# Kernel tuning notes

Measured on AMD Instinct MI355X. Metric: run time of the kernel, lower is better.

The kernel has to match this reference:

```python
import jax, jax.numpy as jnp
import numpy as np
import math

N_NODES = 100000
D = 64
N_EDGES = 1280000
LN_EPS = 1e-5


def setup_inputs() -> dict:
    key = jax.random.key(0)
    ks = jax.random.split(key, 8)
    x = jax.random.normal(ks[0], (N_NODES, D), dtype=jnp.float32)
    edge_index = jax.random.randint(ks[1], (2, N_EDGES), 0, N_NODES, dtype=jnp.int64)
    # xavier_uniform with gain=0.1 for weight matrices
    limit = 0.1 * math.sqrt(6.0 / (D + D))
    qk_w = jax.random.uniform(ks[2], (D, D), dtype=jnp.float32, minval=-limit, maxval=limit)
    v_w = jax.random.uniform(ks[3], (D, D), dtype=jnp.float32, minval=-limit, maxval=limit)
    o_w = jax.random.uniform(ks[4], (D, D), dtype=jnp.float32, minval=-limit, maxval=limit)
    qk_b = jnp.zeros((D,), dtype=jnp.float32)
    v_b = jnp.zeros((D,), dtype=jnp.float32)
    o_b = jnp.zeros((D,), dtype=jnp.float32)
    ln_g = jnp.ones((D,), dtype=jnp.float32)
    ln_b = jnp.zeros((D,), dtype=jnp.float32)
    return {"x": x, "edge_index": edge_index, "qk_w": qk_w, "qk_b": qk_b,
            "v_w": v_w, "v_b": v_b, "o_w": o_w, "o_b": o_b,
            "ln_g": ln_g, "ln_b": ln_b}


def reference(x, edge_index, qk_w, qk_b, v_w, v_b, o_w, o_b, ln_g, ln_b):
    n = x.shape[0]
    # shared Q/K projection and V projection (torch Linear: x @ W^T + b)
    qk = x @ qk_w.T + qk_b            # [N, D]
    v = x @ v_w.T + v_b               # [N, D]

    src = edge_index[0]
    dst = edge_index[1]

    # edge-wise attention logits: <q[dst], k[src]> / sqrt(D), clamped
    scores = jnp.sum(qk[dst] * qk[src], axis=-1) / math.sqrt(v.shape[-1])  # [E]
    scores = jnp.clip(scores, -5.0, 5.0)

    # segment softmax over incoming edges of each destination node
    seg_max = jax.ops.segment_max(scores, dst, num_segments=n)   # [N], -inf for empty
    e = jnp.exp(scores - seg_max[dst])                           # [E]
    seg_sum = jax.ops.segment_sum(e, dst, num_segments=n)        # [N]
    attn = e / seg_sum[dst]                                      # [E]

    # weighted scatter-add aggregation (nodes with no in-edges stay zero)
    out = jax.ops.segment_sum(attn[:, None] * v[src], dst, num_segments=n)  # [N, D]

    out = out @ o_w.T + o_b

    # LayerNorm(out + residual)
    h = out + x
    mu = jnp.mean(h, axis=-1, keepdims=True)
    var = jnp.mean(jnp.square(h - mu), axis=-1, keepdims=True)
    h = (h - mu) * jax.lax.rsqrt(var + LN_EPS)
    return h * ln_g + ln_b
```

## Files before the change

### kernel.cpp

```cpp
#include <hip/hip_runtime.h>
#include <hip/hip_bf16.h>
#include <math.h>

#define DD 64
#define CAP 64
#define BINSZ 256
#define SLOTS 32
#define EPB 2048
#define NBINS 391
#define LN_EPS 1e-5f

typedef float v2f __attribute__((ext_vector_type(2)));
typedef __attribute__((ext_vector_type(8))) short bf16x8;
typedef __attribute__((ext_vector_type(4))) float f32x4;

__device__ __forceinline__ float bf2f(unsigned short u) {
    return __uint_as_float(((unsigned)u) << 16);
}
__device__ __forceinline__ short f2bf(float f) {
    __hip_bfloat16 h = __float2bfloat16(f);
    return *reinterpret_cast<short*>(&h);
}
__device__ __forceinline__ bf16x8 cvt8(const float* p) {
    float4 a = *(const float4*)p;
    float4 b = *(const float4*)(p + 4);
    bf16x8 r;
    r[0] = f2bf(a.x); r[1] = f2bf(a.y); r[2] = f2bf(a.z); r[3] = f2bf(a.w);
    r[4] = f2bf(b.x); r[5] = f2bf(b.y); r[6] = f2bf(b.z); r[7] = f2bf(b.w);
    return r;
}
__device__ __forceinline__ unsigned char f2fp8(float f) {
    return (unsigned char)(__builtin_amdgcn_cvt_pk_fp8_f32(f, 0.f, 0, false) & 0xff);
}

__global__ __launch_bounds__(256) void prep_kernel(
    const float* __restrict__ x,
    const float* __restrict__ qk_w, const float* __restrict__ qk_b,
    const float* __restrict__ v_w,  const float* __restrict__ v_b,
    const int* __restrict__ eidx, int* __restrict__ cnttab,
    unsigned* __restrict__ ebuf,
    __hip_bfloat16* __restrict__ qk, unsigned char* __restrict__ kv,
    int n, int E, int AB)
{
    __shared__ int lhist[NBINS];
    __shared__ unsigned char lkv[64 * 128];
    __shared__ unsigned short lq[64 * 64];

    int bid = blockIdx.x;
    int tid = threadIdx.x;
    if (bid < AB) {
        for (int b = tid; b < NBINS; b += 256) lhist[b] = 0;
        __syncthreads();
        int nv = E >> 2;
        int b4 = (bid * EPB >> 2) + tid;
        const uint4* dst4 = (const uint4*)(eidx + E);
        const uint4* src4 = (const uint4*)(eidx);
        unsigned* slab = ebuf + (size_t)bid * NBINS * SLOTS;
        #pragma unroll
        for (int g = 0; g < 2; ++g) {
            int i4 = b4 + g * 256;
            if (i4 < nv) {
                uint4 d = dst4[i4];
                uint4 s = src4[i4];
                #pragma unroll
                for (int c = 0; c < 4; ++c) {
                    unsigned dd = (c == 0) ? d.x : (c == 1) ? d.y
                                : (c == 2) ? d.z : d.w;
                    unsigned ss = (c == 0) ? s.x : (c == 1) ? s.y
                                : (c == 2) ? s.z : s.w;
                    int bin = dd >> 8;
                    int r = atomicAdd(&lhist[bin], 1);
                    if (r < SLOTS)
                        slab[bin * SLOTS + r] = (ss << 8) | (dd & 255);
                }
            }
        }
        __syncthreads();
        int* mycnt = cnttab + bid * NBINS;
        for (int b = tid; b < NBINS; b += 256)
            mycnt[b] = min(lhist[b], SLOTS);
    } else {
        int pbid = bid - AB;
        int wave = tid >> 6, lane = tid & 63;
        int node0 = pbid * 64 + wave * 16;
        int lr = lane & 15;
        int lk = (lane >> 4) << 3;

        if (node0 < n) {
            int arow = min(node0 + lr, n - 1);
            const float* xr = x + (size_t)arow * 64 + lk;
            bf16x8 A0 = cvt8(xr);
            bf16x8 A1 = cvt8(xr + 32);

            float qbias[4] = {qk_b[lr], qk_b[16 + lr], qk_b[32 + lr], qk_b[48 + lr]};
            float vbias[4] = {v_b[lr],  v_b[16 + lr],  v_b[32 + lr],  v_b[48 + lr]};

            f32x4 z = {0.f, 0.f, 0.f, 0.f};
            f32x4 accq[4], accv[4];
            #pragma unroll
            for (int ct = 0; ct < 4; ++ct) {
                const float* wq = qk_w + (size_t)(ct * 16 + lr) * 64 + lk;
                bf16x8 Bq0 = cvt8(wq);
                bf16x8 Bq1 = cvt8(wq + 32);
                f32x4 aq = __builtin_amdgcn_mfma_f32_16x16x32_bf16(A0, Bq0, z, 0, 0, 0);
                aq = __builtin_amdgcn_mfma_f32_16x16x32_bf16(A1, Bq1, aq, 0, 0, 0);
                accq[ct] = aq;
                const float* wv = v_w + (size_t)(ct * 16 + lr) * 64 + lk;
                bf16x8 Bv0 = cvt8(wv);
                bf16x8 Bv1 = cvt8(wv + 32);
                f32x4 av = __builtin_amdgcn_mfma_f32_16x16x32_bf16(A0, Bv0, z, 0, 0, 0);
                av = __builtin_amdgcn_mfma_f32_16x16x32_bf16(A1, Bv1, av, 0, 0, 0);
                accv[ct] = av;
            }
            #pragma unroll
            for (int ct = 0; ct < 4; ++ct) {
                int dim  = ct * 16 + lr;
                int koff = ((dim >> 2) << 3) + (dim & 3);
                #pragma unroll
                for (int r = 0; r < 4; ++r) {
                    int ndl = wave * 16 + ((lane >> 4) << 2) + r;
                    float q = accq[ct][r] + qbias[ct];
                    float v = accv[ct][r] + vbias[ct];
                    lq[ndl * 64 + dim] = (unsigned short)f2bf(q);
                    lkv[ndl * 128 + koff]     = f2fp8(q);
                    lkv[ndl * 128 + koff + 4] = f2fp8(v);
                }
            }
        }
        __syncthreads();
        int row = tid >> 2;
        size_t gnode = (size_t)pbid * 64 + row;
        if (gnode < (size_t)n) {
            const uint4* skv = (const uint4*)(lkv + tid * 32);
            uint4* dkv = (uint4*)(kv + (size_t)pbid * 64 * 128 + tid * 32);
            dkv[0] = skv[0];
            dkv[1] = skv[1];
            const uint4* sq = (const uint4*)((const unsigned char*)lq + tid * 32);
            uint4* dq = (uint4*)((unsigned char*)qk + (size_t)pbid * 64 * 128 + tid * 32);
            dq[0] = sq[0];
            dq[1] = sq[1];
        }
    }
}

__global__ __launch_bounds__(256) void bucket_kernel(
    const int* __restrict__ cnttab, const unsigned* __restrict__ ebuf,
    int* __restrict__ deg, int* __restrict__ bucket, int n, int NPB)
{
    __shared__ int lbkt[BINSZ * CAP];
    __shared__ int ldeg[BINSZ];
    int bin = blockIdx.x, tid = threadIdx.x;
    ldeg[tid] = 0;
    __syncthreads();
    for (int c = tid; c < NPB; c += 256) {
        int cnt = cnttab[c * NBINS + bin];
        const unsigned* run = ebuf + ((size_t)c * NBINS + bin) * SLOTS;
        for (int r = 0; r < cnt; ++r) {
            unsigned e = run[r];
            int rel = e & 255;
            int rr = atomicAdd(&ldeg[rel], 1);
            if (rr < CAP) lbkt[(rel << 6) + rr] = (int)(e >> 8);
        }
    }
    __syncthreads();
    size_t gbase = (size_t)(bin << 8) << 6;
    int node0 = bin << 8;
    for (int i = tid; i < BINSZ * CAP; i += 256) {
        if (node0 + (i >> 6) < n) bucket[gbase + i] = lbkt[i];
    }
    int node = node0 + tid;
    if (node < n) deg[node] = min(ldeg[tid], CAP);
}

__global__ __launch_bounds__(256) void attn_kernel(
    const __hip_bfloat16* __restrict__ qk, const unsigned char* __restrict__ kv,
    const int* __restrict__ deg, const int* __restrict__ bucket,
    __hip_bfloat16* __restrict__ outd, int n)
{
    int tid = threadIdx.x;
    int wave = tid >> 6, lane = tid & 63;
    int node = blockIdx.x * 4 + wave;
    if (node >= n) return;

    int sub = lane >> 4;
    int sl  = lane & 15;

    ushort4 qu = *(const ushort4*)(qk + ((size_t)node << 6) + (sl << 2));
    float4 q4 = make_float4(bf2f(qu.x), bf2f(qu.y), bf2f(qu.z), bf2f(qu.w));
    int dn = deg[node];
    int medge = bucket[((size_t)node << 6) + lane];

    float s = 0.f;
    float4 acc = {0.f, 0.f, 0.f, 0.f};
    const float ESCALE = 0.18033688f;

    for (int base = 0; base < dn; base += 16) {
        int m1 = dn - 1;
        int i0 = base + sub;
        int i1 = i0 + 4, i2 = i0 + 8, i3 = i0 + 12;
        int s0 = __shfl(medge, min(i0, m1));
        int s1 = __shfl(medge, min(i1, m1));
        int s2 = __shfl(medge, min(i2, m1));
        int s3 = __shfl(medge, min(i3, m1));
        uint2 w0 = *(const uint2*)(kv + ((unsigned)s0 << 7) + (sl << 3));
        uint2 w1 = *(const uint2*)(kv + ((unsigned)s1 << 7) + (sl << 3));
        uint2 w2 = *(const uint2*)(kv + ((unsigned)s2 << 7) + (sl << 3));
        uint2 w3 = *(const uint2*)(kv + ((unsigned)s3 << 7) + (sl << 3));
        v2f k0l = __builtin_amdgcn_cvt_pk_f32_fp8(w0.x, false);
        v2f k0h = __builtin_amdgcn_cvt_pk_f32_fp8(w0.x, true);
        v2f k1l = __builtin_amdgcn_cvt_pk_f32_fp8(w1.x, false);
        v2f k1h = __builtin_amdgcn_cvt_pk_f32_fp8(w1.x, true);
        v2f k2l = __builtin_amdgcn_cvt_pk_f32_fp8(w2.x, false);
        v2f k2h = __builtin_amdgcn_cvt_pk_f32_fp8(w2.x, true);
        v2f k3l = __builtin_amdgcn_cvt_pk_f32_fp8(w3.x, false);
        v2f k3h = __builtin_amdgcn_cvt_pk_f32_fp8(w3.x, true);
        float p0 = q4.x*k0l.x + q4.y*k0l.y + q4.z*k0h.x + q4.w*k0h.y;
        float p1 = q4.x*k1l.x + q4.y*k1l.y + q4.z*k1h.x + q4.w*k1h.y;
        float p2 = q4.x*k2l.x + q4.y*k2l.y + q4.z*k2h.x + q4.w*k2h.y;
        float p3 = q4.x*k3l.x + q4.y*k3l.y + q4.z*k3h.x + q4.w*k3h.y;
        #pragma unroll
        for (int w = 1; w <= 8; w <<= 1) {
            p0 += __shfl_xor(p0, w); p1 += __shfl_xor(p1, w);
            p2 += __shfl_xor(p2, w); p3 += __shfl_xor(p3, w);
        }
        float pe0 = (i0 < dn) ? __builtin_amdgcn_exp2f(p0 * ESCALE) : 0.f;
        float pe1 = (i1 < dn) ? __builtin_amdgcn_exp2f(p1 * ESCALE) : 0.f;
        float pe2 = (i2 < dn) ? __builtin_amdgcn_exp2f(p2 * ESCALE) : 0.f;
        float pe3 = (i3 < dn) ? __builtin_amdgcn_exp2f(p3 * ESCALE) : 0.f;
        s += (pe0 + pe1) + (pe2 + pe3);
        v2f v0l = __builtin_amdgcn_cvt_pk_f32_fp8(w0.y, false);
        v2f v0h = __builtin_amdgcn_cvt_pk_f32_fp8(w0.y, true);
        v2f v1l = __builtin_amdgcn_cvt_pk_f32_fp8(w1.y, false);
        v2f v1h = __builtin_amdgcn_cvt_pk_f32_fp8(w1.y, true);
        v2f v2l = __builtin_amdgcn_cvt_pk_f32_fp8(w2.y, false);
        v2f v2h = __builtin_amdgcn_cvt_pk_f32_fp8(w2.y, true);
        v2f v3l = __builtin_amdgcn_cvt_pk_f32_fp8(w3.y, false);
        v2f v3h = __builtin_amdgcn_cvt_pk_f32_fp8(w3.y, true);
        acc.x += (pe0 * v0l.x + pe1 * v1l.x) + (pe2 * v2l.x + pe3 * v3l.x);
        acc.y += (pe0 * v0l.y + pe1 * v1l.y) + (pe2 * v2l.y + pe3 * v3l.y);
        acc.z += (pe0 * v0h.x + pe1 * v1h.x) + (pe2 * v2h.x + pe3 * v3h.x);
        acc.w += (pe0 * v0h.y + pe1 * v1h.y) + (pe2 * v2h.y + pe3 * v3h.y);
    }

    s += __shfl_xor(s, 16); s += __shfl_xor(s, 32);
    acc.x += __shfl_xor(acc.x, 16); acc.x += __shfl_xor(acc.x, 32);
    acc.y += __shfl_xor(acc.y, 16); acc.y += __shfl_xor(acc.y, 32);
    acc.z += __shfl_xor(acc.z, 16); acc.z += __shfl_xor(acc.z, 32);
    acc.w += __shfl_xor(acc.w, 16); acc.w += __shfl_xor(acc.w, 32);

    float inv = (dn > 0) ? (1.0f / s) : 0.f;
    if (sub == 0) {
        ushort4 o;
        o.x = (unsigned short)f2bf(acc.x * inv);
        o.y = (unsigned short)f2bf(acc.y * inv);
        o.z = (unsigned short)f2bf(acc.z * inv);
        o.w = (unsigned short)f2bf(acc.w * inv);
        *(ushort4*)(outd + ((size_t)node << 6) + (sl << 2)) = o;
    }
}

__global__ __launch_bounds__(256) void epi_kernel(
    const __hip_bfloat16* __restrict__ outd, const float* __restrict__ x,
    const float* __restrict__ o_w, const float* __restrict__ o_b,
    const float* __restrict__ ln_g, const float* __restrict__ ln_b,
    float* __restrict__ out, int n)
{
    int tid = threadIdx.x;
    int wave = tid >> 6, lane = tid & 63;
    int node0 = blockIdx.x * 64 + wave * 16;
    if (node0 >= n) return;

    int lr = lane & 15;
    int lk = (lane >> 4) << 3;

    int arow = min(node0 + lr, n - 1);
    const __hip_bfloat16* odr = outd + (size_t)arow * 64 + lk;
    bf16x8 A0 = *(const bf16x8*)odr;
    bf16x8 A1 = *(const bf16x8*)(odr + 32);

    f32x4 z = {0.f, 0.f, 0.f, 0.f};
    f32x4 acc[4];
    #pragma unroll
    for (int ct = 0; ct < 4; ++ct) {
        const float* wo = o_w + (size_t)(ct * 16 + lr) * 64 + lk;
        bf16x8 B0 = cvt8(wo);
        bf16x8 B1 = cvt8(wo + 32);
        f32x4 a = __builtin_amdgcn_mfma_f32_16x16x32_bf16(A0, B0, z, 0, 0, 0);
        a = __builtin_amdgcn_mfma_f32_16x16x32_bf16(A1, B1, a, 0, 0, 0);
        acc[ct] = a;
    }
    float ob[4] = {o_b[lr], o_b[16 + lr], o_b[32 + lr], o_b[48 + lr]};
    float lg[4] = {ln_g[lr], ln_g[16 + lr], ln_g[32 + lr], ln_g[48 + lr]};
    float lb[4] = {ln_b[lr], ln_b[16 + lr], ln_b[32 + lr], ln_b[48 + lr]};

    #pragma unroll
    for (int r = 0; r < 4; ++r) {
        int nd = node0 + ((lane >> 4) << 2) + r;
        if (nd >= n) break;
        float h[4];
        #pragma unroll
        for (int ct = 0; ct < 4; ++ct)
            h[ct] = acc[ct][r] + ob[ct] + x[(size_t)nd * 64 + ct * 16 + lr];
        float m = (h[0] + h[1]) + (h[2] + h[3]);
        #pragma unroll
        for (int w = 1; w <= 8; w <<= 1) m += __shfl_xor(m, w);
        m *= (1.f / 64.f);
        float d0 = h[0] - m, d1 = h[1] - m, d2 = h[2] - m, d3 = h[3] - m;
        float vv = (d0 * d0 + d1 * d1) + (d2 * d2 + d3 * d3);
        #pragma unroll
        for (int w = 1; w <= 8; w <<= 1) vv += __shfl_xor(vv, w);
        vv *= (1.f / 64.f);
        float rs = rsqrtf(vv + LN_EPS);
        float* op = out + (size_t)nd * 64 + lr;
        op[0]  = d0 * rs * lg[0] + lb[0];
        op[16] = d1 * rs * lg[1] + lb[1];
        op[32] = d2 * rs * lg[2] + lb[2];
        op[48] = d3 * rs * lg[3] + lb[3];
    }
}

extern "C" void kernel_launch(void* const* d_in, const int* in_sizes, int n_in,
                              void* d_out, int out_size, void* d_ws, size_t ws_size,
                              hipStream_t stream)
{
    const float* x    = (const float*)d_in[0];
    const int*   eidx = (const int*)  d_in[1];
    const float* qk_w = (const float*)d_in[2];
    const float* qk_b = (const float*)d_in[3];
    const float* v_w  = (const float*)d_in[4];
    const float* v_b  = (const float*)d_in[5];
    const float* o_w  = (const float*)d_in[6];
    const float* o_b  = (const float*)d_in[7];
    const float* ln_g = (const float*)d_in[8];
    const float* ln_b = (const float*)d_in[9];

    const int n = in_sizes[0] / DD;
    const int E = in_sizes[1] / 2;
    const int AB = (E + EPB - 1) / EPB;
    const int PB = (n + 63) / 64;

    char* ws = (char*)d_ws;
    size_t off = 0;
    __hip_bfloat16* qk = (__hip_bfloat16*)(ws + off); off += (size_t)n * 64 * 2;
    unsigned char* kv  = (unsigned char*)(ws + off); off += (size_t)n * 128;
    int* deg    = (int*)(ws + off); off += (size_t)n * 4;
    int* bucket = (int*)(ws + off); off += (size_t)n * CAP * 4;
    int* cnttab = (int*)(ws + off); off += (size_t)AB * NBINS * 4;
    unsigned* ebuf = (unsigned*)(ws + off); off += (size_t)AB * NBINS * SLOTS * 4;
    __hip_bfloat16* outd = (__hip_bfloat16*)(ws + off); off += (size_t)n * 64 * 2;

    prep_kernel<<<AB + PB, 256, 0, stream>>>(x, qk_w, qk_b, v_w, v_b,
                                             eidx, cnttab, ebuf, qk, kv, n, E, AB);
    bucket_kernel<<<NBINS, 256, 0, stream>>>(cnttab, ebuf, deg, bucket, n, AB);
    attn_kernel<<<(n + 3) / 4, 256, 0, stream>>>(qk, kv, deg, bucket, outd, n);
    epi_kernel<<<(n + 63) / 64, 256, 0, stream>>>(outd, x, o_w, o_b, ln_g, ln_b,
                                                  (float*)d_out, n);
}
```

Measured before the change: 129.2 us.

## Fuse attention aggregation with output projection and LayerNorm epilogue

Merges the per-node attention kernel into the epilogue kernel. Each wave now processes 16 nodes sequentially and stages the aggregated bf16 rows in shared memory for the MFMA projection and LayerNorm. This removes the intermediate global buffer round trip and one kernel launch. In exchange, the grid becomes much smaller and each wave handles its nodes serially, which reduces parallelism for latency-bound gathers.

```diff
diff --git a/kernel.cpp b/kernel.cpp
--- a/kernel.cpp
+++ b/kernel.cpp
@@ -175,108 +175,100 @@
 __global__ __launch_bounds__(256) void attn_kernel(
     const __hip_bfloat16* __restrict__ qk, const unsigned char* __restrict__ kv,
     const int* __restrict__ deg, const int* __restrict__ bucket,
-    __hip_bfloat16* __restrict__ outd, int n)
-{
-    int tid = threadIdx.x;
-    int wave = tid >> 6, lane = tid & 63;
-    int node = blockIdx.x * 4 + wave;
-    if (node >= n) return;
-
-    int sub = lane >> 4;
-    int sl  = lane & 15;
-
-    ushort4 qu = *(const ushort4*)(qk + ((size_t)node << 6) + (sl << 2));
-    float4 q4 = make_float4(bf2f(qu.x), bf2f(qu.y), bf2f(qu.z), bf2f(qu.w));
-    int dn = deg[node];
-    int medge = bucket[((size_t)node << 6) + lane];
-
-    float s = 0.f;
-    float4 acc = {0.f, 0.f, 0.f, 0.f};
-    const float ESCALE = 0.18033688f;
-
-    for (int base = 0; base < dn; base += 16) {
-        int m1 = dn - 1;
-        int i0 = base + sub;
-        int i1 = i0 + 4, i2 = i0 + 8, i3 = i0 + 12;
-        int s0 = __shfl(medge, min(i0, m1));
-        int s1 = __shfl(medge, min(i1, m1));
-        int s2 = __shfl(medge, min(i2, m1));
-        int s3 = __shfl(medge, min(i3, m1));
-        uint2 w0 = *(const uint2*)(kv + ((unsigned)s0 << 7) + (sl << 3));
-        uint2 w1 = *(const uint2*)(kv + ((unsigned)s1 << 7) + (sl << 3));
-        uint2 w2 = *(const uint2*)(kv + ((unsigned)s2 << 7) + (sl << 3));
-        uint2 w3 = *(const uint2*)(kv + ((unsigned)s3 << 7) + (sl << 3));
-        v2f k0l = __builtin_amdgcn_cvt_pk_f32_fp8(w0.x, false);
-        v2f k0h = __builtin_amdgcn_cvt_pk_f32_fp8(w0.x, true);
-        v2f k1l = __builtin_amdgcn_cvt_pk_f32_fp8(w1.x, false);
-        v2f k1h = __builtin_amdgcn_cvt_pk_f32_fp8(w1.x, true);
-        v2f k2l = __builtin_amdgcn_cvt_pk_f32_fp8(w2.x, false);
-        v2f k2h = __builtin_amdgcn_cvt_pk_f32_fp8(w2.x, true);
-        v2f k3l = __builtin_amdgcn_cvt_pk_f32_fp8(w3.x, false);
-        v2f k3h = __builtin_amdgcn_cvt_pk_f32_fp8(w3.x, true);
-        float p0 = q4.x*k0l.x + q4.y*k0l.y + q4.z*k0h.x + q4.w*k0h.y;
-        float p1 = q4.x*k1l.x + q4.y*k1l.y + q4.z*k1h.x + q4.w*k1h.y;
-        float p2 = q4.x*k2l.x + q4.y*k2l.y + q4.z*k2h.x + q4.w*k2h.y;
-        float p3 = q4.x*k3l.x + q4.y*k3l.y + q4.z*k3h.x + q4.w*k3h.y;
-        #pragma unroll
-        for (int w = 1; w <= 8; w <<= 1) {
-            p0 += __shfl_xor(p0, w); p1 += __shfl_xor(p1, w);
-            p2 += __shfl_xor(p2, w); p3 += __shfl_xor(p3, w);
-        }
-        float pe0 = (i0 < dn) ? __builtin_amdgcn_exp2f(p0 * ESCALE) : 0.f;
-        float pe1 = (i1 < dn) ? __builtin_amdgcn_exp2f(p1 * ESCALE) : 0.f;
-        float pe2 = (i2 < dn) ? __builtin_amdgcn_exp2f(p2 * ESCALE) : 0.f;
-        float pe3 = (i3 < dn) ? __builtin_amdgcn_exp2f(p3 * ESCALE) : 0.f;
-        s += (pe0 + pe1) + (pe2 + pe3);
-        v2f v0l = __builtin_amdgcn_cvt_pk_f32_fp8(w0.y, false);
-        v2f v0h = __builtin_amdgcn_cvt_pk_f32_fp8(w0.y, true);
-        v2f v1l = __builtin_amdgcn_cvt_pk_f32_fp8(w1.y, false);
-        v2f v1h = __builtin_amdgcn_cvt_pk_f32_fp8(w1.y, true);
-        v2f v2l = __builtin_amdgcn_cvt_pk_f32_fp8(w2.y, false);
-        v2f v2h = __builtin_amdgcn_cvt_pk_f32_fp8(w2.y, true);
-        v2f v3l = __builtin_amdgcn_cvt_pk_f32_fp8(w3.y, false);
-        v2f v3h = __builtin_amdgcn_cvt_pk_f32_fp8(w3.y, true);
-        acc.x += (pe0 * v0l.x + pe1 * v1l.x) + (pe2 * v2l.x + pe3 * v3l.x);
-        acc.y += (pe0 * v0l.y + pe1 * v1l.y) + (pe2 * v2l.y + pe3 * v3l.y);
-        acc.z += (pe0 * v0h.x + pe1 * v1h.x) + (pe2 * v2h.x + pe3 * v3h.x);
-        acc.w += (pe0 * v0h.y + pe1 * v1h.y) + (pe2 * v2h.y + pe3 * v3h.y);
-    }
-
-    s += __shfl_xor(s, 16); s += __shfl_xor(s, 32);
-    acc.x += __shfl_xor(acc.x, 16); acc.x += __shfl_xor(acc.x, 32);
-    acc.y += __shfl_xor(acc.y, 16); acc.y += __shfl_xor(acc.y, 32);
-    acc.z += __shfl_xor(acc.z, 16); acc.z += __shfl_xor(acc.z, 32);
-    acc.w += __shfl_xor(acc.w, 16); acc.w += __shfl_xor(acc.w, 32);
-
-    float inv = (dn > 0) ? (1.0f / s) : 0.f;
-    if (sub == 0) {
-        ushort4 o;
-        o.x = (unsigned short)f2bf(acc.x * inv);
-        o.y = (unsigned short)f2bf(acc.y * inv);
-        o.z = (unsigned short)f2bf(acc.z * inv);
-        o.w = (unsigned short)f2bf(acc.w * inv);
-        *(ushort4*)(outd + ((size_t)node << 6) + (sl << 2)) = o;
-    }
-}
-
-__global__ __launch_bounds__(256) void epi_kernel(
-    const __hip_bfloat16* __restrict__ outd, const float* __restrict__ x,
+    const float* __restrict__ x,
     const float* __restrict__ o_w, const float* __restrict__ o_b,
     const float* __restrict__ ln_g, const float* __restrict__ ln_b,
     float* __restrict__ out, int n)
 {
+    __shared__ __hip_bfloat16 lodb[4][16][64];
     int tid = threadIdx.x;
     int wave = tid >> 6, lane = tid & 63;
-    int node0 = blockIdx.x * 64 + wave * 16;
-    if (node0 >= n) return;
-
+    int nbase = blockIdx.x * 64 + wave * 16;
+    int sub = lane >> 4;
+    int sl  = lane & 15;
+    const float ESCALE = 0.18033688f;
+
+    for (int k = 0; k < 16; ++k) {
+        int node = nbase + k;
+        bool valid = node < n;
+        int nc = valid ? node : (n - 1);
+        ushort4 qu = *(const ushort4*)(qk + ((size_t)nc << 6) + (sl << 2));
+        float4 q4 = make_float4(bf2f(qu.x), bf2f(qu.y), bf2f(qu.z), bf2f(qu.w));
+        int dn = valid ? deg[node] : 0;
+        int medge = bucket[((size_t)nc << 6) + lane];
+
+        float s = 0.f;
+        float4 acc = {0.f, 0.f, 0.f, 0.f};
+        for (int base = 0; base < dn; base += 16) {
+            int m1 = dn - 1;
+            int i0 = base + sub;
+            int i1 = i0 + 4, i2 = i0 + 8, i3 = i0 + 12;
+            int s0 = __shfl(medge, min(i0, m1));
+            int s1 = __shfl(medge, min(i1, m1));
+            int s2 = __shfl(medge, min(i2, m1));
+            int s3 = __shfl(medge, min(i3, m1));
+            uint2 w0 = *(const uint2*)(kv + ((unsigned)s0 << 7) + (sl << 3));
+            uint2 w1 = *(const uint2*)(kv + ((unsigned)s1 << 7) + (sl << 3));
+            uint2 w2 = *(const uint2*)(kv + ((unsigned)s2 << 7) + (sl << 3));
+            uint2 w3 = *(const uint2*)(kv + ((unsigned)s3 << 7) + (sl << 3));
+            v2f k0l = __builtin_amdgcn_cvt_pk_f32_fp8(w0.x, false);
+            v2f k0h = __builtin_amdgcn_cvt_pk_f32_fp8(w0.x, true);
+            v2f k1l = __builtin_amdgcn_cvt_pk_f32_fp8(w1.x, false);
+            v2f k1h = __builtin_amdgcn_cvt_pk_f32_fp8(w1.x, true);
+            v2f k2l = __builtin_amdgcn_cvt_pk_f32_fp8(w2.x, false);
+            v2f k2h = __builtin_amdgcn_cvt_pk_f32_fp8(w2.x, true);
+            v2f k3l = __builtin_amdgcn_cvt_pk_f32_fp8(w3.x, false);
+            v2f k3h = __builtin_amdgcn_cvt_pk_f32_fp8(w3.x, true);
+            float p0 = q4.x*k0l.x + q4.y*k0l.y + q4.z*k0h.x + q4.w*k0h.y;
+            float p1 = q4.x*k1l.x + q4.y*k1l.y + q4.z*k1h.x + q4.w*k1h.y;
+            float p2 = q4.x*k2l.x + q4.y*k2l.y + q4.z*k2h.x + q4.w*k2h.y;
+            float p3 = q4.x*k3l.x + q4.y*k3l.y + q4.z*k3h.x + q4.w*k3h.y;
+            #pragma unroll
+            for (int w = 1; w <= 8; w <<= 1) {
+                p0 += __shfl_xor(p0, w); p1 += __shfl_xor(p1, w);
+                p2 += __shfl_xor(p2, w); p3 += __shfl_xor(p3, w);
+            }
+            float pe0 = (i0 < dn) ? __builtin_amdgcn_exp2f(p0 * ESCALE) : 0.f;
+            float pe1 = (i1 < dn) ? __builtin_amdgcn_exp2f(p1 * ESCALE) : 0.f;
+            float pe2 = (i2 < dn) ? __builtin_amdgcn_exp2f(p2 * ESCALE) : 0.f;
+            float pe3 = (i3 < dn) ? __builtin_amdgcn_exp2f(p3 * ESCALE) : 0.f;
+            s += (pe0 + pe1) + (pe2 + pe3);
+            v2f v0l = __builtin_amdgcn_cvt_pk_f32_fp8(w0.y, false);
+            v2f v0h = __builtin_amdgcn_cvt_pk_f32_fp8(w0.y, true);
+            v2f v1l = __builtin_amdgcn_cvt_pk_f32_fp8(w1.y, false);
+            v2f v1h = __builtin_amdgcn_cvt_pk_f32_fp8(w1.y, true);
+            v2f v2l = __builtin_amdgcn_cvt_pk_f32_fp8(w2.y, false);
+            v2f v2h = __builtin_amdgcn_cvt_pk_f32_fp8(w2.y, true);
+            v2f v3l = __builtin_amdgcn_cvt_pk_f32_fp8(w3.y, false);
+            v2f v3h = __builtin_amdgcn_cvt_pk_f32_fp8(w3.y, true);
+            acc.x += (pe0 * v0l.x + pe1 * v1l.x) + (pe2 * v2l.x + pe3 * v3l.x);
+            acc.y += (pe0 * v0l.y + pe1 * v1l.y) + (pe2 * v2l.y + pe3 * v3l.y);
+            acc.z += (pe0 * v0h.x + pe1 * v1h.x) + (pe2 * v2h.x + pe3 * v3h.x);
+            acc.w += (pe0 * v0h.y + pe1 * v1h.y) + (pe2 * v2h.y + pe3 * v3h.y);
+        }
+        s += __shfl_xor(s, 16); s += __shfl_xor(s, 32);
+        acc.x += __shfl_xor(acc.x, 16); acc.x += __shfl_xor(acc.x, 32);
+        acc.y += __shfl_xor(acc.y, 16); acc.y += __shfl_xor(acc.y, 32);
+        acc.z += __shfl_xor(acc.z, 16); acc.z += __shfl_xor(acc.z, 32);
+        acc.w += __shfl_xor(acc.w, 16); acc.w += __shfl_xor(acc.w, 32);
+
+        float inv = (dn > 0) ? (1.0f / s) : 0.f;
+        if (sub == 0) {
+            ushort4 o;
+            o.x = (unsigned short)f2bf(acc.x * inv);
+            o.y = (unsigned short)f2bf(acc.y * inv);
+            o.z = (unsigned short)f2bf(acc.z * inv);
+            o.w = (unsigned short)f2bf(acc.w * inv);
+            *(ushort4*)&lodb[wave][k][sl << 2] = o;
+        }
+    }
+
+    if (nbase >= n) return;
     int lr = lane & 15;
     int lk = (lane >> 4) << 3;
 
-    int arow = min(node0 + lr, n - 1);
-    const __hip_bfloat16* odr = outd + (size_t)arow * 64 + lk;
-    bf16x8 A0 = *(const bf16x8*)odr;
-    bf16x8 A1 = *(const bf16x8*)(odr + 32);
+    bf16x8 A0 = *(const bf16x8*)&lodb[wave][lr][lk];
+    bf16x8 A1 = *(const bf16x8*)&lodb[wave][lr][lk + 32];
 
     f32x4 z = {0.f, 0.f, 0.f, 0.f};
     f32x4 acc[4];
@@ -295,7 +287,7 @@
 
     #pragma unroll
     for (int r = 0; r < 4; ++r) {
-        int nd = node0 + ((lane >> 4) << 2) + r;
+        int nd = nbase + ((lane >> 4) << 2) + r;
         if (nd >= n) break;
         float h[4];
         #pragma unroll
@@ -347,12 +339,11 @@
     int* bucket = (int*)(ws + off); off += (size_t)n * CAP * 4;
     int* cnttab = (int*)(ws + off); off += (size_t)AB * NBINS * 4;
     unsigned* ebuf = (unsigned*)(ws + off); off += (size_t)AB * NBINS * SLOTS * 4;
-    __hip_bfloat16* outd = (__hip_bfloat16*)(ws + off); off += (size_t)n * 64 * 2;
 
     prep_kernel<<<AB + PB, 256, 0, stream>>>(x, qk_w, qk_b, v_w, v_b,
                                              eidx, cnttab, ebuf, qk, kv, n, E, AB);
     bucket_kernel<<<NBINS, 256, 0, stream>>>(cnttab, ebuf, deg, bucket, n, AB);
-    attn_kernel<<<(n + 3) / 4, 256, 0, stream>>>(qk, kv, deg, bucket, outd, n);
-    epi_kernel<<<(n + 63) / 64, 256, 0, stream>>>(outd, x, o_w, o_b, ln_g, ln_b,
-                                                  (float*)d_out, n);
-}
+    attn_kernel<<<(n + 63) / 64, 256, 0, stream>>>(qk, kv, deg, bucket, x,
+                                                   o_w, o_b, ln_g, ln_b,
+                                                   (float*)d_out, n);
+}
```

Result: slower. 138.8 us (+7.4%).
